# Kernel tuning notes

Measured on AMD Instinct MI355X. Metric: run time of the kernel, lower is better.

Reference implementation:

```python
import jax, jax.numpy as jnp
import numpy as np

N, D_IN, D_H, D_OUT, E = 32768, 1024, 2048, 1024, 8

def setup_inputs() -> dict:
    key = jax.random.key(0)
    ks = jax.random.split(key, 8)
    s_in = 1.0 / np.sqrt(D_IN)
    s_h = 1.0 / np.sqrt(D_H)
    return {
        "x": jax.random.normal(ks[0], (N, D_IN), dtype=jnp.float32),
        "Wr": jax.random.normal(ks[1], (D_IN, E), dtype=jnp.float32) * s_in,
        "br": jnp.zeros((E,), dtype=jnp.float32),
        "W1": jax.random.normal(ks[2], (E, D_IN, D_H), dtype=jnp.float32) * s_in,
        "b1": jnp.zeros((E, D_H), dtype=jnp.float32),
        "W2": jax.random.normal(ks[3], (E, D_H, D_OUT), dtype=jnp.float32) * s_h,
        "b2": jnp.zeros((E, D_OUT), dtype=jnp.float32),
    }

def reference(x, Wr, br, W1, b1, W2, b2):
    # Supervised router: encoder is Identity, router is Linear + softmax.
    router_probs = jax.nn.softmax(x @ Wr + br, axis=-1)            # [N, E]
    router_probs_max = jnp.max(router_probs, axis=-1)              # [N]
    routes = jnp.argmax(router_probs, axis=-1)                     # [N] int
    counts = jnp.sum(jax.nn.one_hot(routes, E, dtype=x.dtype), axis=0)  # [E]

    # Top-1 dispatch: each token goes through exactly one expert MLP.
    # Small fixed loop over experts (E=8); mask-combine replaces gather/scatter.
    out = jnp.zeros((N, D_OUT), dtype=x.dtype)
    for e in range(E):
        h = jax.nn.relu(x @ W1[e] + b1[e])                         # [N, D_H]
        y = h @ W2[e] + b2[e]                                      # [N, D_OUT]
        out = out + jnp.where((routes == e)[:, None], y, jnp.zeros((), x.dtype))
    # Straight-through scaling: value 1 in fwd, routes grad through router prob.
    scale = router_probs_max / jax.lax.stop_gradient(router_probs_max)
    out = out * scale[:, None]
    return out, router_probs, counts
```

## Files before the change

kernel.cpp:

```cpp
#include <hip/hip_runtime.h>
#include <stdint.h>


#define NTOK   32768
#define DIN    1024
#define DH     2048
#define DOUT   1024
#define NEXP   8

typedef unsigned short u16;
typedef __bf16 bf16x8 __attribute__((ext_vector_type(8)));
typedef float  f32x4  __attribute__((ext_vector_type(4)));
typedef unsigned short us8 __attribute__((ext_vector_type(8)));
typedef const __attribute__((address_space(1))) void gvoid_t;
typedef __attribute__((address_space(3))) void svoid_t;

__device__ __forceinline__ u16 f2bf(float f) {
  union { float f; uint32_t u; } v; v.f = f;
  return (u16)((v.u + 0x7FFFu + ((v.u >> 16) & 1u)) >> 16);
}

__global__ __launch_bounds__(256) void k_router(
    const float* __restrict__ x, const float* __restrict__ Wr,
    const float* __restrict__ br, float* __restrict__ probs,
    int* __restrict__ routes, u16* __restrict__ xb)
{
  __shared__ float wr_s[NEXP * DIN];
  int tid = threadIdx.x;
  for (int idx = tid; idx < DIN * NEXP / 4; idx += 256) {
    float4 v = ((const float4*)Wr)[idx];
    int k = idx >> 1, r = (idx & 1) * 4;
    wr_s[(r + 0) * DIN + k] = v.x;
    wr_s[(r + 1) * DIN + k] = v.y;
    wr_s[(r + 2) * DIN + k] = v.z;
    wr_s[(r + 3) * DIN + k] = v.w;
  }
  __syncthreads();
  int lane = tid & 63, wv = tid >> 6;
  int t = blockIdx.x * 4 + wv;
  const float* xr = x + (size_t)t * DIN;
  u16* xbrow = xb + (size_t)t * DIN;
  float acc[NEXP];
  #pragma unroll
  for (int e = 0; e < NEXP; ++e) acc[e] = 0.f;
  #pragma unroll
  for (int i = 0; i < 4; ++i) {
    int k = i * 256 + lane * 4;
    float4 xv = *(const float4*)(xr + k);
    ushort4 o;
    o.x = f2bf(xv.x); o.y = f2bf(xv.y); o.z = f2bf(xv.z); o.w = f2bf(xv.w);
    *(ushort4*)(xbrow + k) = o;
    #pragma unroll
    for (int e = 0; e < NEXP; ++e) {
      float4 w4 = *(const float4*)(wr_s + e * DIN + k);
      acc[e] += xv.x * w4.x + xv.y * w4.y + xv.z * w4.z + xv.w * w4.w;
    }
  }
  #pragma unroll
  for (int off = 32; off >= 1; off >>= 1) {
    #pragma unroll
    for (int e = 0; e < NEXP; ++e) acc[e] += __shfl_xor(acc[e], off, 64);
  }
  if (lane == 0) {
    float l[NEXP], m = -1e30f;
    #pragma unroll
    for (int e = 0; e < NEXP; ++e) { l[e] = acc[e] + br[e]; m = fmaxf(m, l[e]); }
    float p[NEXP], s = 0.f;
    #pragma unroll
    for (int e = 0; e < NEXP; ++e) { p[e] = expf(l[e] - m); s += p[e]; }
    float inv = 1.f / s;
    int am = 0; float best = l[0];
    #pragma unroll
    for (int e = 1; e < NEXP; ++e) if (l[e] > best) { best = l[e]; am = e; }
    float4 pa = {p[0] * inv, p[1] * inv, p[2] * inv, p[3] * inv};
    float4 pb = {p[4] * inv, p[5] * inv, p[6] * inv, p[7] * inv};
    float4* pd = (float4*)(probs + (size_t)t * NEXP);
    pd[0] = pa; pd[1] = pb;
    routes[t] = am;
  }
}

__global__ __launch_bounds__(256) void k_count(
    const int* __restrict__ routes, int* __restrict__ aux)
{
  int t = blockIdx.x * 256 + threadIdx.x;
  int e = routes[t];
  int lane = threadIdx.x & 63;
  #pragma unroll
  for (int ee = 0; ee < NEXP; ++ee) {
    unsigned long long m = __ballot(e == ee);
    if (lane == 0 && m) atomicAdd(&aux[ee], (int)__popcll(m));
  }
}

__global__ __launch_bounds__(256) void k_prefix(int* __restrict__ aux, float* __restrict__ counts_out)
{
  __shared__ int s_off[NEXP], s_cnt[NEXP], s_tb[NEXP], s_nt;
  int tid = threadIdx.x;
  if (tid == 0) {
    int off = 0, tb = 0;
    for (int e = 0; e < NEXP; ++e) {
      int c = aux[e];
      counts_out[e] = (float)c;
      s_cnt[e] = c; s_off[e] = off; s_tb[e] = tb;
      aux[24 + e] = off;
      off += c; tb += (c + 127) >> 7;
    }
    s_nt = tb;
    aux[16] = tb;
  }
  __syncthreads();
  int nt = s_nt;
  for (int i = tid; i < nt; i += 256) {
    int e = 0;
    #pragma unroll
    for (int k = 1; k < NEXP; ++k) if (i >= s_tb[k]) e = k;
    int tt = i - s_tb[e];
    aux[128 + i] = e;
    aux[512 + i] = s_off[e] + tt * 128;
    aux[896 + i] = s_off[e] + s_cnt[e];
  }
}

__global__ __launch_bounds__(256) void k_assign(
    const int* __restrict__ routes, int* __restrict__ aux,
    int* __restrict__ tok_of_pos)
{
  int t = blockIdx.x * 256 + threadIdx.x;
  int e = routes[t];
  int lane = threadIdx.x & 63;
  int p = 0;
  #pragma unroll
  for (int ee = 0; ee < NEXP; ++ee) {
    unsigned long long m = __ballot(e == ee);
    int base = 0;
    if (lane == 0 && m) base = atomicAdd(&aux[8 + ee], (int)__popcll(m));
    base = __shfl(base, 0, 64);
    if (e == ee)
      p = aux[24 + ee] + base + (int)__popcll(m & ((1ull << lane) - 1ull));
  }
  tok_of_pos[p] = t;
}

__global__ __launch_bounds__(256) void k_transpose(
    const float* __restrict__ W1, u16* __restrict__ W1t,
    const float* __restrict__ W2, u16* __restrict__ W2t)
{
  int z = blockIdx.z;
  const float* src; u16* dst; int K, Nn, e;
  if (z < NEXP) { src = W1; dst = W1t; K = DIN; Nn = DH;   e = z; }
  else          { src = W2; dst = W2t; K = DH;  Nn = DOUT; e = z - NEXP; }
  int k0 = blockIdx.x * 64, n0 = blockIdx.y * 64;
  if (k0 >= K || n0 >= Nn) return;
  __shared__ float tile[64][65];
  const float* s = src + ((size_t)e * K + k0) * Nn + n0;
  int r = threadIdx.x >> 6, c = threadIdx.x & 63;
  #pragma unroll
  for (int i = 0; i < 16; ++i)
    tile[r + i * 4][c] = s[(size_t)(r + i * 4) * Nn + c];
  __syncthreads();
  u16* d = dst + ((size_t)e * Nn + n0) * K + k0;
  int kg = (threadIdx.x & 7) * 8, nr0 = threadIdx.x >> 3;
  #pragma unroll
  for (int p = 0; p < 2; ++p) {
    int nr = nr0 + p * 32;
    us8 o;
    #pragma unroll
    for (int j = 0; j < 8; ++j) o[j] = f2bf(tile[kg + j][nr]);
    *(us8*)(d + (size_t)nr * K + kg) = o;
  }
}

template<int MODE, int GATHER>
__global__ __launch_bounds__(256, 4) void k_gemm(
    const u16* __restrict__ A, const u16* __restrict__ Bt,
    const float* __restrict__ bias, u16* __restrict__ Hout,
    float* __restrict__ Yout, const int* __restrict__ tok_of_pos,
    const int* __restrict__ aux, int K, int Nn, int nbyl)
{
  int nwg = gridDim.x;
  int bid = blockIdx.x;
  int wg  = (bid & 7) * (nwg >> 3) + (bid >> 3);
  int by  = wg & ((1 << nbyl) - 1);
  int bx  = wg >> nbyl;
  if (bx >= aux[16]) return;
  int e  = aux[128 + bx];
  int r0 = aux[512 + bx];
  int r1 = aux[896 + bx];
  int bn0 = by << 7;

  __shared__ __align__(16) u16 As[128 * 64];
  __shared__ __align__(16) u16 Bs[128 * 64];

  int tid = threadIdx.x;
  int lane = tid & 63, wv = tid >> 6;
  int wr = wv >> 1, wc = wv & 1;
  const u16* Be = Bt + (size_t)e * Nn * K;

  int tk[4];
  #pragma unroll
  for (int r = 0; r < 4; ++r) {
    int gr = r0 + r * 32 + (tid >> 3);
    gr = gr < NTOK ? gr : NTOK - 1;
    tk[r] = GATHER ? tok_of_pos[gr] : gr;
  }

  auto stage = [&](int kt) {
    int k0 = kt * 64;
    #pragma unroll
    for (int r = 0; r < 4; ++r) {
      int L = (r * 256 + tid) * 16;
      int sl = ((L >> 4) & 7) ^ ((L >> 7) & 7);
      __builtin_amdgcn_global_load_lds(
          (gvoid_t*)((const char*)(A + (size_t)tk[r] * K + k0) + sl * 16),
          (svoid_t*)((char*)As + L), 16, 0, 0);
    }
    #pragma unroll
    for (int r = 0; r < 4; ++r) {
      int L = (r * 256 + tid) * 16;
      int row = L >> 7;
      int sl = ((L >> 4) & 7) ^ (row & 7);
      __builtin_amdgcn_global_load_lds(
          (gvoid_t*)((const char*)(Be + (size_t)(bn0 + row) * K + k0) + sl * 16),
          (svoid_t*)((char*)Bs + L), 16, 0, 0);
    }
  };

  f32x4 acc[4][4];
  #pragma unroll
  for (int i = 0; i < 4; ++i)
    #pragma unroll
    for (int j = 0; j < 4; ++j)
      acc[i][j] = (f32x4){0.f, 0.f, 0.f, 0.f};

  int KT = K >> 6;
  stage(0);
  for (int kt = 0; kt < KT; ++kt) {
    __syncthreads();
    const char* As_c = (const char*)As;
    const char* Bs_c = (const char*)Bs;
    #pragma unroll
    for (int kk = 0; kk < 2; ++kk) {
      int sw = ((kk * 4 + (lane >> 4)) ^ (lane & 7)) << 4;
      bf16x8 a[4], b[4];
      #pragma unroll
      for (int f = 0; f < 4; ++f)
        a[f] = *(const bf16x8*)(As_c + (wr * 64 + f * 16 + (lane & 15)) * 128 + sw);
      #pragma unroll
      for (int f = 0; f < 4; ++f)
        b[f] = *(const bf16x8*)(Bs_c + (wc * 64 + f * 16 + (lane & 15)) * 128 + sw);
      #pragma unroll
      for (int i = 0; i < 4; ++i)
        #pragma unroll
        for (int j = 0; j < 4; ++j)
          acc[i][j] = __builtin_amdgcn_mfma_f32_16x16x32_bf16(a[i], b[j], acc[i][j], 0, 0, 0);
    }
    __syncthreads();
    if (kt + 1 < KT) stage(kt + 1);
  }

  const float* be = bias + (size_t)e * Nn;
  float bv[4];
  #pragma unroll
  for (int j = 0; j < 4; ++j) bv[j] = be[bn0 + wc * 64 + j * 16 + (lane & 15)];
  #pragma unroll
  for (int i = 0; i < 4; ++i) {
    #pragma unroll
    for (int q = 0; q < 4; ++q) {
      int r = r0 + wr * 64 + i * 16 + (lane >> 4) * 4 + q;
      if (r < r1) {
        if (MODE == 0) {
          u16* dst = Hout + (size_t)r * Nn + bn0 + wc * 64 + (lane & 15);
          #pragma unroll
          for (int j = 0; j < 4; ++j)
            dst[j * 16] = f2bf(fmaxf(acc[i][j][q] + bv[j], 0.f));
        } else {
          int tok = tok_of_pos[r];
          float* dst = Yout + (size_t)tok * Nn + bn0 + wc * 64 + (lane & 15);
          #pragma unroll
          for (int j = 0; j < 4; ++j)
            dst[j * 16] = acc[i][j][q] + bv[j];
        }
      }
    }
  }
}

extern "C" void kernel_launch(void* const* d_in, const int* in_sizes, int n_in,
                              void* d_out, int out_size, void* d_ws, size_t ws_size,
                              hipStream_t stream)
{
  const float* x  = (const float*)d_in[0];
  const float* Wr = (const float*)d_in[1];
  const float* br = (const float*)d_in[2];
  const float* W1 = (const float*)d_in[3];
  const float* b1 = (const float*)d_in[4];
  const float* W2 = (const float*)d_in[5];
  const float* b2 = (const float*)d_in[6];

  float* out    = (float*)d_out;
  float* probs  = out + (size_t)NTOK * DOUT;
  float* counts = probs + (size_t)NTOK * NEXP;

  char* ws = (char*)d_ws;
  u16* xb          = (u16*)(ws);
  u16* h           = (u16*)(ws + 67108864);
  u16* W1t         = (u16*)(ws + 201326592);
  u16* W2t         = (u16*)(ws + 234881024);
  int* aux         = (int*)(ws + 268435456);
  int* routes      = (int*)(ws + 268451840);
  int* tok_of_pos  = (int*)(ws + 268582912);

  (void)hipMemsetAsync(aux, 0, 16384, stream);
  k_router<<<NTOK / 4, 256, 0, stream>>>(x, Wr, br, probs, routes, xb);
  k_count<<<NTOK / 256, 256, 0, stream>>>(routes, aux);
  k_transpose<<<dim3(32, 32, 2 * NEXP), 256, 0, stream>>>(W1, W1t, W2, W2t);
  k_prefix<<<1, 256, 0, stream>>>(aux, counts);
  k_assign<<<NTOK / 256, 256, 0, stream>>>(routes, aux, tok_of_pos);
  k_gemm<0, 1><<<264 * 16, 256, 0, stream>>>(xb, W1t, b1, h, nullptr, tok_of_pos, aux, DIN, DH, 4);
  k_gemm<1, 0><<<264 * 8, 256, 0, stream>>>(h, W2t, b2, nullptr, out, tok_of_pos, aux, DH, DOUT, 3);
}
```

Baseline: 526.6 us.

## Fuse expert counting into router and load GEMM A operand directly to registers

The router kernel now processes 16 tokens per wave and builds a per-block shared histogram of routes, which it adds atomically to the global counts. This removes the separate counting kernel and reduces the number of Wr shared-memory loads. The GEMM no longer stages the A tile in LDS; each lane loads its bf16x8 A fragments straight from global memory, with a per-row gathered pointer. Occupancy hint drops from 4 to 3 blocks per CU, giving more registers in exchange for uncoalesced, unpipelined A loads that are duplicated across the two column waves.

```diff
diff --git a/kernel.cpp b/kernel.cpp
--- a/kernel.cpp
+++ b/kernel.cpp
@@ -23,10 +23,12 @@
 __global__ __launch_bounds__(256) void k_router(
     const float* __restrict__ x, const float* __restrict__ Wr,
     const float* __restrict__ br, float* __restrict__ probs,
-    int* __restrict__ routes, u16* __restrict__ xb)
+    int* __restrict__ routes, u16* __restrict__ xb, int* __restrict__ aux)
 {
   __shared__ float wr_s[NEXP * DIN];
+  __shared__ int hist[NEXP];
   int tid = threadIdx.x;
+  if (tid < NEXP) hist[tid] = 0;
   for (int idx = tid; idx < DIN * NEXP / 4; idx += 256) {
     float4 v = ((const float4*)Wr)[idx];
     int k = idx >> 1, r = (idx & 1) * 4;
@@ -37,60 +39,53 @@
   }
   __syncthreads();
   int lane = tid & 63, wv = tid >> 6;
-  int t = blockIdx.x * 4 + wv;
-  const float* xr = x + (size_t)t * DIN;
-  u16* xbrow = xb + (size_t)t * DIN;
-  float acc[NEXP];
-  #pragma unroll
-  for (int e = 0; e < NEXP; ++e) acc[e] = 0.f;
-  #pragma unroll
-  for (int i = 0; i < 4; ++i) {
-    int k = i * 256 + lane * 4;
-    float4 xv = *(const float4*)(xr + k);
-    ushort4 o;
-    o.x = f2bf(xv.x); o.y = f2bf(xv.y); o.z = f2bf(xv.z); o.w = f2bf(xv.w);
-    *(ushort4*)(xbrow + k) = o;
-    #pragma unroll
-    for (int e = 0; e < NEXP; ++e) {
-      float4 w4 = *(const float4*)(wr_s + e * DIN + k);
-      acc[e] += xv.x * w4.x + xv.y * w4.y + xv.z * w4.z + xv.w * w4.w;
-    }
-  }
-  #pragma unroll
-  for (int off = 32; off >= 1; off >>= 1) {
-    #pragma unroll
-    for (int e = 0; e < NEXP; ++e) acc[e] += __shfl_xor(acc[e], off, 64);
-  }
-  if (lane == 0) {
-    float l[NEXP], m = -1e30f;
-    #pragma unroll
-    for (int e = 0; e < NEXP; ++e) { l[e] = acc[e] + br[e]; m = fmaxf(m, l[e]); }
-    float p[NEXP], s = 0.f;
-    #pragma unroll
-    for (int e = 0; e < NEXP; ++e) { p[e] = expf(l[e] - m); s += p[e]; }
-    float inv = 1.f / s;
-    int am = 0; float best = l[0];
-    #pragma unroll
-    for (int e = 1; e < NEXP; ++e) if (l[e] > best) { best = l[e]; am = e; }
-    float4 pa = {p[0] * inv, p[1] * inv, p[2] * inv, p[3] * inv};
-    float4 pb = {p[4] * inv, p[5] * inv, p[6] * inv, p[7] * inv};
-    float4* pd = (float4*)(probs + (size_t)t * NEXP);
-    pd[0] = pa; pd[1] = pb;
-    routes[t] = am;
-  }
-}
-
-__global__ __launch_bounds__(256) void k_count(
-    const int* __restrict__ routes, int* __restrict__ aux)
-{
-  int t = blockIdx.x * 256 + threadIdx.x;
-  int e = routes[t];
-  int lane = threadIdx.x & 63;
-  #pragma unroll
-  for (int ee = 0; ee < NEXP; ++ee) {
-    unsigned long long m = __ballot(e == ee);
-    if (lane == 0 && m) atomicAdd(&aux[ee], (int)__popcll(m));
-  }
+  int base = (blockIdx.x * 4 + wv) * 16;
+  for (int it = 0; it < 16; ++it) {
+    int t = base + it;
+    const float* xr = x + (size_t)t * DIN;
+    u16* xbrow = xb + (size_t)t * DIN;
+    float acc[NEXP];
+    #pragma unroll
+    for (int e = 0; e < NEXP; ++e) acc[e] = 0.f;
+    #pragma unroll
+    for (int i = 0; i < 4; ++i) {
+      int k = i * 256 + lane * 4;
+      float4 xv = *(const float4*)(xr + k);
+      ushort4 o;
+      o.x = f2bf(xv.x); o.y = f2bf(xv.y); o.z = f2bf(xv.z); o.w = f2bf(xv.w);
+      *(ushort4*)(xbrow + k) = o;
+      #pragma unroll
+      for (int e = 0; e < NEXP; ++e) {
+        float4 w4 = *(const float4*)(wr_s + e * DIN + k);
+        acc[e] += xv.x * w4.x + xv.y * w4.y + xv.z * w4.z + xv.w * w4.w;
+      }
+    }
+    #pragma unroll
+    for (int off = 32; off >= 1; off >>= 1) {
+      #pragma unroll
+      for (int e = 0; e < NEXP; ++e) acc[e] += __shfl_xor(acc[e], off, 64);
+    }
+    if (lane == 0) {
+      float l[NEXP], m = -1e30f;
+      #pragma unroll
+      for (int e = 0; e < NEXP; ++e) { l[e] = acc[e] + br[e]; m = fmaxf(m, l[e]); }
+      float p[NEXP], s = 0.f;
+      #pragma unroll
+      for (int e = 0; e < NEXP; ++e) { p[e] = expf(l[e] - m); s += p[e]; }
+      float inv = 1.f / s;
+      int am = 0; float best = l[0];
+      #pragma unroll
+      for (int e = 1; e < NEXP; ++e) if (l[e] > best) { best = l[e]; am = e; }
+      float4 pa = {p[0] * inv, p[1] * inv, p[2] * inv, p[3] * inv};
+      float4 pb = {p[4] * inv, p[5] * inv, p[6] * inv, p[7] * inv};
+      float4* pd = (float4*)(probs + (size_t)t * NEXP);
+      pd[0] = pa; pd[1] = pb;
+      routes[t] = am;
+      atomicAdd(&hist[am], 1);
+    }
+  }
+  __syncthreads();
+  if (tid < NEXP && hist[tid]) atomicAdd(&aux[tid], hist[tid]);
 }
 
 __global__ __launch_bounds__(256) void k_prefix(int* __restrict__ aux, float* __restrict__ counts_out)
@@ -172,7 +167,7 @@
 }
 
 template<int MODE, int GATHER>
-__global__ __launch_bounds__(256, 4) void k_gemm(
+__global__ __launch_bounds__(256, 3) void k_gemm(
     const u16* __restrict__ A, const u16* __restrict__ Bt,
     const float* __restrict__ bias, u16* __restrict__ Hout,
     float* __restrict__ Yout, const int* __restrict__ tok_of_pos,
@@ -189,7 +184,6 @@
   int r1 = aux[896 + bx];
   int bn0 = by << 7;
 
-  __shared__ __align__(16) u16 As[128 * 64];
   __shared__ __align__(16) u16 Bs[128 * 64];
 
   int tid = threadIdx.x;
@@ -197,24 +191,17 @@
   int wr = wv >> 1, wc = wv & 1;
   const u16* Be = Bt + (size_t)e * Nn * K;
 
-  int tk[4];
-  #pragma unroll
-  for (int r = 0; r < 4; ++r) {
-    int gr = r0 + r * 32 + (tid >> 3);
+  const u16* Ap[4];
+  #pragma unroll
+  for (int f = 0; f < 4; ++f) {
+    int gr = r0 + wr * 64 + f * 16 + (lane & 15);
     gr = gr < NTOK ? gr : NTOK - 1;
-    tk[r] = GATHER ? tok_of_pos[gr] : gr;
-  }
-
-  auto stage = [&](int kt) {
+    int tk = GATHER ? tok_of_pos[gr] : gr;
+    Ap[f] = A + (size_t)tk * K + ((lane >> 4) * 8);
+  }
+
+  auto stageB = [&](int kt) {
     int k0 = kt * 64;
-    #pragma unroll
-    for (int r = 0; r < 4; ++r) {
-      int L = (r * 256 + tid) * 16;
-      int sl = ((L >> 4) & 7) ^ ((L >> 7) & 7);
-      __builtin_amdgcn_global_load_lds(
-          (gvoid_t*)((const char*)(A + (size_t)tk[r] * K + k0) + sl * 16),
-          (svoid_t*)((char*)As + L), 16, 0, 0);
-    }
     #pragma unroll
     for (int r = 0; r < 4; ++r) {
       int L = (r * 256 + tid) * 16;
@@ -234,18 +221,21 @@
       acc[i][j] = (f32x4){0.f, 0.f, 0.f, 0.f};
 
   int KT = K >> 6;
-  stage(0);
+  stageB(0);
   for (int kt = 0; kt < KT; ++kt) {
+    bf16x8 a[4][2];
+    #pragma unroll
+    for (int f = 0; f < 4; ++f) {
+      #pragma unroll
+      for (int kk = 0; kk < 2; ++kk)
+        a[f][kk] = *(const bf16x8*)(Ap[f] + kt * 64 + kk * 32);
+    }
     __syncthreads();
-    const char* As_c = (const char*)As;
     const char* Bs_c = (const char*)Bs;
     #pragma unroll
     for (int kk = 0; kk < 2; ++kk) {
       int sw = ((kk * 4 + (lane >> 4)) ^ (lane & 7)) << 4;
-      bf16x8 a[4], b[4];
-      #pragma unroll
-      for (int f = 0; f < 4; ++f)
-        a[f] = *(const bf16x8*)(As_c + (wr * 64 + f * 16 + (lane & 15)) * 128 + sw);
+      bf16x8 b[4];
       #pragma unroll
       for (int f = 0; f < 4; ++f)
         b[f] = *(const bf16x8*)(Bs_c + (wc * 64 + f * 16 + (lane & 15)) * 128 + sw);
@@ -253,10 +243,10 @@
       for (int i = 0; i < 4; ++i)
         #pragma unroll
         for (int j = 0; j < 4; ++j)
-          acc[i][j] = __builtin_amdgcn_mfma_f32_16x16x32_bf16(a[i], b[j], acc[i][j], 0, 0, 0);
+          acc[i][j] = __builtin_amdgcn_mfma_f32_16x16x32_bf16(a[i][kk], b[j], acc[i][j], 0, 0, 0);
     }
     __syncthreads();
-    if (kt + 1 < KT) stage(kt + 1);
+    if (kt + 1 < KT) stageB(kt + 1);
   }
 
   const float* be = bias + (size_t)e * Nn;
@@ -312,8 +302,7 @@
   int* tok_of_pos  = (int*)(ws + 268582912);
 
   (void)hipMemsetAsync(aux, 0, 16384, stream);
-  k_router<<<NTOK / 4, 256, 0, stream>>>(x, Wr, br, probs, routes, xb);
-  k_count<<<NTOK / 256, 256, 0, stream>>>(routes, aux);
+  k_router<<<NTOK / 64, 256, 0, stream>>>(x, Wr, br, probs, routes, xb, aux);
   k_transpose<<<dim3(32, 32, 2 * NEXP), 256, 0, stream>>>(W1, W1t, W2, W2t);
   k_prefix<<<1, 256, 0, stream>>>(aux, counts);
   k_assign<<<NTOK / 256, 256, 0, stream>>>(routes, aux, tok_of_pos);
```

Result: slower. 787.1 us (+49.5%).
